# Kernel tuning notes

Hardware: AMD Instinct MI355X
Metric: run time of the kernel (lower is better)

The kernel has to match this reference:

```python
import jax, jax.numpy as jnp
import numpy as np

B, T, C = 2, 2048, 1024
E, F = 8, 1024        # n_experts, expert ffn dim
FS = 2048             # shared expert ffn dim
TOP_K = 2


def setup_inputs() -> dict:
    key = jax.random.key(0)
    ks = jax.random.split(key, 6)
    s = lambda *d: 1.0 / np.sqrt(d[-1])
    return {
        "hidden_tensor": jax.random.normal(ks[0], (B, T, C), jnp.float32),
        "w_router": jax.random.normal(ks[1], (E, C), jnp.float32) * s(C),
        "w1_stack": jax.random.normal(ks[2], (E, F, C), jnp.float32) * s(C),
        "w2_stack": jax.random.normal(ks[3], (E, C, F), jnp.float32) * s(F),
        "ws1": jax.random.normal(ks[4], (FS, C), jnp.float32) * s(C),
        "ws2": jax.random.normal(ks[5], (C, FS), jnp.float32) * s(FS),
    }


def reference(hidden_tensor, w_router, w1_stack, w2_stack, ws1, ws2):
    Bb, Tt, Cc = hidden_tensor.shape
    x = hidden_tensor.reshape(-1, Cc)                      # (t, C)
    t = x.shape[0]

    # --- router: softmax over experts, top-k, renormalize ---
    logits = x @ w_router.T                                # (t, E)
    probs = jax.nn.softmax(logits, axis=-1)
    expert_weight, expert_idx = jax.lax.top_k(probs, TOP_K)  # (t, k)
    expert_weight = expert_weight / jnp.sum(expert_weight, axis=-1, keepdims=True)

    # --- dispatch: stable sort token-expert pairs by expert id ---
    flat_e = expert_idx.reshape(-1)                        # (t*k,)
    order = jnp.argsort(flat_e, stable=True)
    sorted_e = flat_e[order]
    flat_tok = jnp.repeat(jnp.arange(t), TOP_K)
    sorted_tok = flat_tok[order]
    sorted_w = expert_weight.reshape(-1)[order]

    counts = jnp.bincount(sorted_e, length=E)              # (E,)
    offsets = jnp.concatenate([jnp.zeros((1,), counts.dtype), jnp.cumsum(counts)])
    local_pos = jnp.arange(t * TOP_K) - offsets[sorted_e]  # position within expert bin

    cap = t * TOP_K  # static capacity (>= true cnt_max), padding rows stay zero
    binned = jnp.zeros((E, cap, Cc), x.dtype).at[sorted_e, local_pos].set(x[sorted_tok])

    # --- grouped expert FFN with squared-ReLU ---
    inter = jnp.einsum('ecd,efd->ecf', binned, w1_stack)   # (E, cap, F)
    inter = jnp.square(jax.nn.relu(inter))
    outb = jnp.einsum('ecf,edf->ecd', inter, w2_stack)     # (E, cap, C)

    # --- combine: gather back, weight, scatter-add to tokens ---
    flat_out = outb[sorted_e, local_pos] * sorted_w[:, None]
    moe_out = jnp.zeros((t, Cc), x.dtype).at[sorted_tok].add(flat_out)
    moe_out = moe_out.reshape(Bb, Tt, Cc)

    # --- shared expert on residual (squared-ReLU MLP) ---
    sh = jnp.square(jax.nn.relu(jnp.einsum('btc,fc->btf', hidden_tensor, ws1)))
    shared_out = jnp.einsum('btf,cf->btc', sh, ws2)

    return shared_out + moe_out
```

## Files before the change

### kernel.cpp

```cpp
#include <hip/hip_runtime.h>
#include <math.h>

typedef unsigned short u16;
typedef unsigned int u32;

typedef __attribute__((ext_vector_type(8))) short bf16x8;
typedef __attribute__((ext_vector_type(4))) float f32x4;

__device__ __forceinline__ u16 f2bf(float f) {
  union { float f; u32 u; } v; v.f = f;
  u32 r = v.u + 0x7FFFu + ((v.u >> 16) & 1u);
  return (u16)(r >> 16);
}
__device__ __forceinline__ float bf2f(u16 h) {
  union { u32 u; float f; } v; v.u = ((u32)h) << 16; return v.f;
}

typedef const u32 __attribute__((address_space(1)))* gas1_t;
typedef u32 __attribute__((address_space(3)))* las3_t;

__device__ __forceinline__ void gload16(const void* g, void* l) {
  __builtin_amdgcn_global_load_lds((gas1_t)g, (las3_t)l, 16, 0, 0);
}

struct Tile { int kind; int g0; int n0; int e; };

__global__ __launch_bounds__(256) void convert_weights(
    const float4* __restrict__ w1, const float4* __restrict__ w2,
    const float4* __restrict__ s1, const float4* __restrict__ s2,
    ushort4* __restrict__ o1, ushort4* __restrict__ o2,
    ushort4* __restrict__ o3, ushort4* __restrict__ o4) {
  size_t i = (size_t)blockIdx.x * 256 + threadIdx.x;
  const size_t n1 = 2097152, n2 = 2097152, n3 = 524288;
  float4 v; ushort4* o; size_t j;
  if (i < n1)              { v = w1[i];            o = o1; j = i; }
  else if (i < n1+n2)      { v = w2[i-n1];         o = o2; j = i-n1; }
  else if (i < n1+n2+n3)   { v = s1[i-n1-n2];      o = o3; j = i-n1-n2; }
  else                     { v = s2[i-n1-n2-n3];   o = o4; j = i-n1-n2-n3; }
  ushort4 r; r.x = f2bf(v.x); r.y = f2bf(v.y); r.z = f2bf(v.z); r.w = f2bf(v.w);
  o[j] = r;
}

__global__ __launch_bounds__(256) void router_kernel(
    const float* __restrict__ x, const float* __restrict__ wr,
    u16* __restrict__ xb, int* __restrict__ tokE, float* __restrict__ tokW) {
  const int wv = threadIdx.x >> 6, lane = threadIdx.x & 63;
  const int tok = blockIdx.x * 4 + wv;
  const float4* xp = (const float4*)(x + (size_t)tok * 1024);
  float4 xv[4];
#pragma unroll
  for (int i = 0; i < 4; ++i) xv[i] = xp[i * 64 + lane];
  ushort4* xo = (ushort4*)xb + (size_t)tok * 256;
#pragma unroll
  for (int i = 0; i < 4; ++i) {
    ushort4 o;
    o.x = f2bf(xv[i].x); o.y = f2bf(xv[i].y); o.z = f2bf(xv[i].z); o.w = f2bf(xv[i].w);
    xo[i * 64 + lane] = o;
  }
  float acc[8];
#pragma unroll
  for (int e = 0; e < 8; ++e) acc[e] = 0.f;
#pragma unroll
  for (int e = 0; e < 8; ++e) {
    const float4* wp = (const float4*)(wr + e * 1024);
#pragma unroll
    for (int i = 0; i < 4; ++i) {
      float4 w4 = wp[i * 64 + lane];
      acc[e] += xv[i].x * w4.x + xv[i].y * w4.y + xv[i].z * w4.z + xv[i].w * w4.w;
    }
  }
#pragma unroll
  for (int m = 32; m > 0; m >>= 1)
#pragma unroll
    for (int e = 0; e < 8; ++e) acc[e] += __shfl_xor(acc[e], m, 64);
  if (lane == 0) {
    int e0 = 0;
#pragma unroll
    for (int e = 1; e < 8; ++e) if (acc[e] > acc[e0]) e0 = e;
    int e1 = (e0 == 0) ? 1 : 0;
#pragma unroll
    for (int e = 0; e < 8; ++e) if (e != e0 && acc[e] > acc[e1]) e1 = e;
    float p1 = __expf(acc[e1] - acc[e0]);
    float w1 = p1 / (1.f + p1);
    float w0 = 1.f - w1;
    tokE[tok * 2] = e0; tokE[tok * 2 + 1] = e1;
    tokW[tok * 2] = w0; tokW[tok * 2 + 1] = w1;
  }
}

__global__ __launch_bounds__(256) void plan_kernel(
    const int* __restrict__ tokE, const float* __restrict__ tokW,
    Tile* __restrict__ upT, Tile* __restrict__ downT,
    int* __restrict__ rowtok, float* __restrict__ roww, int* __restrict__ invrow) {
  const int t = threadIdx.x, lane = t & 63, wv = t >> 6;
  int myE[32];
#pragma unroll
  for (int i = 0; i < 32; ++i) myE[i] = tokE[t * 32 + i];
  int lcnt[8] = {};
#pragma unroll
  for (int i = 0; i < 32; ++i) ++lcnt[myE[i]];

  __shared__ int wtot[8][4];
  __shared__ int aoffS[9];
  __shared__ int etile[72 * 2];
  int excl[8];
#pragma unroll
  for (int e = 0; e < 8; ++e) {
    int v = lcnt[e];
#pragma unroll
    for (int off = 1; off < 64; off <<= 1) {
      int n = __shfl_up(v, (unsigned)off, 64);
      if (lane >= off) v += n;
    }
    if (lane == 63) wtot[e][wv] = v;
    excl[e] = v - lcnt[e];
  }
  __syncthreads();
#pragma unroll
  for (int e = 0; e < 8; ++e)
    for (int w = 0; w < wv; ++w) excl[e] += wtot[e][w];

  if (t == 0) {
    int s = 0, ti = 0;
    for (int e = 0; e < 8; ++e) {
      aoffS[e] = s;
      int cnt = wtot[e][0] + wtot[e][1] + wtot[e][2] + wtot[e][3];
      int tiles = (cnt + 127) >> 7;
      for (int k = 0; k < tiles; ++k) { etile[2 * ti] = e; etile[2 * ti + 1] = s + k * 128; ++ti; }
      s += tiles << 7;
    }
    aoffS[8] = s;
    for (; ti < 72; ++ti) { etile[2 * ti] = -1; etile[2 * ti + 1] = 0; }
  }
  for (int i = t; i < 9216; i += 256) { rowtok[i] = 0; roww[i] = 0.f; }
  __syncthreads();

  for (int i = t; i < 1088; i += 256) {
    int x = i & 7, s = i >> 3;
    Tile tl;
    if (s < 64) {
      int gg = x & 3, nn = x >> 2;
      int gl = s & 7, nl = s >> 3;
      tl.kind = 0; tl.g0 = (gg * 8 + gl) * 128; tl.n0 = (nn * 8 + nl) * 128; tl.e = 0;
    } else {
      int s2_ = s - 64;
      int mg = x & 3, ng = x >> 2;
      int ml = s2_ % 18, nl = s2_ / 18;
      int mi = mg * 18 + ml;
      int e = etile[2 * mi];
      tl.kind = (e < 0) ? -1 : 1; tl.g0 = etile[2 * mi + 1];
      tl.n0 = (ng * 4 + nl) * 128; tl.e = (e < 0) ? 0 : e;
    }
    upT[i] = tl;
  }
  for (int i = t; i < 832; i += 256) {
    int x = i & 7, s = i >> 3;
    Tile tl;
    if (s < 32) {
      int gg = x & 3, nn = x >> 2;
      int gl = s & 7, nl = s >> 3;
      tl.kind = 0; tl.g0 = (gg * 8 + gl) * 128; tl.n0 = (nn * 4 + nl) * 128; tl.e = 0;
    } else {
      int s2_ = s - 32;
      int mg = x & 3, ng = x >> 2;
      int ml = s2_ % 18, nl = s2_ / 18;
      int mi = mg * 18 + ml;
      int e = etile[2 * mi];
      tl.kind = (e < 0) ? -1 : 1; tl.g0 = etile[2 * mi + 1];
      tl.n0 = (ng * 4 + nl) * 128; tl.e = (e < 0) ? 0 : e;
    }
    downT[i] = tl;
  }

  int pos[8];
#pragma unroll
  for (int e = 0; e < 8; ++e) pos[e] = aoffS[e] + excl[e];
#pragma unroll
  for (int i = 0; i < 32; ++i) {
    int idx = t * 32 + i;
    int e = myE[i];
    int g = pos[e]++;
    rowtok[g] = idx >> 1;
    roww[g] = tokW[idx];
    invrow[idx] = g;
  }
}

__global__ __launch_bounds__(256) void combine_kernel(
    const u16* __restrict__ Ym, const int* __restrict__ invrow,
    const float* __restrict__ tokW, float* __restrict__ out) {
  const int t = blockIdx.x;
  const int r0 = invrow[2 * t], r1 = invrow[2 * t + 1];
  const float w0 = tokW[2 * t], w1 = tokW[2 * t + 1];
  const ushort4* y0 = (const ushort4*)(Ym + (size_t)r0 * 1024);
  const ushort4* y1 = (const ushort4*)(Ym + (size_t)r1 * 1024);
  float4* o = (float4*)(out + (size_t)t * 1024);
  const int c = threadIdx.x;
  ushort4 a = y0[c], b = y1[c];
  float4 v = o[c];
  v.x += w0 * bf2f(a.x) + w1 * bf2f(b.x);
  v.y += w0 * bf2f(a.y) + w1 * bf2f(b.y);
  v.z += w0 * bf2f(a.z) + w1 * bf2f(b.z);
  v.w += w0 * bf2f(a.w) + w1 * bf2f(b.w);
  o[c] = v;
}

template <int PHASE>
__global__ __launch_bounds__(256)
void gemm_fused(const Tile* __restrict__ tiles,
                const u16* __restrict__ A0, const u16* __restrict__ B0, void* __restrict__ C0,
                const u16* __restrict__ A1, const u16* __restrict__ B1, void* __restrict__ C1,
                const int* __restrict__ rowtok, const float* __restrict__ roww) {
  __shared__ u16 As[128 * 64];
  __shared__ u16 Bs[128 * 64];

  Tile tm = tiles[blockIdx.x];
  if (tm.kind < 0) return;
  if (PHASE == 2 && tm.kind != 0) return;
  if (PHASE == 3 && tm.kind != 1) return;

  const int tid = threadIdx.x;
  const int lane = tid & 63;
  const int wv = tid >> 6;
  const int wrow = wv >> 1, wcol = wv & 1;

  const u16* A; const u16* B; void* C; int N, K;
  if (tm.kind == 0) {
    A = A0; B = B0; C = C0;
    N = (PHASE == 0) ? 2048 : 1024;
    K = (PHASE == 0) ? 1024 : 2048;
  } else {
    A = A1; B = B1 + ((size_t)tm.e << 20); C = (PHASE == 3) ? C0 : C1;
    N = 1024; K = 1024;
  }
  const int g0 = tm.g0, n0 = tm.n0;

  const u16* aSrc[4];
  const u16* bSrc[4];
  u32 ldsOff[4];
#pragma unroll
  for (int p = 0; p < 4; ++p) {
    int c = p * 256 + tid;
    int row = c >> 3, slot = c & 7;
    int q = (slot - (row >> 1) - 4 * (row & 1)) & 7;
    int arow = g0 + row;
    if (PHASE == 0 && tm.kind == 1) arow = rowtok[arow];
    aSrc[p] = A + (size_t)arow * K + q * 8;
    bSrc[p] = B + (size_t)(n0 + row) * K + q * 8;
    ldsOff[p] = (u32)(p * 256 + wv * 64) * 16u;
  }

  const int fr = lane & 15, fq = lane >> 4;
  const int swBase = (fr >> 1) + 4 * (fr & 1);
  const int sw0 = ((fq + swBase) & 7) * 8;
  const int sw1 = ((fq + 4 + swBase) & 7) * 8;
  const int aRow = (wrow * 64 + fr) * 64;
  const int bRow = (wcol * 64 + fr) * 64;

  f32x4 acc[4][4] = {};

  for (int k0 = 0; k0 < K; k0 += 64) {
#pragma unroll
    for (int p = 0; p < 4; ++p) {
      gload16(aSrc[p] + k0, (char*)As + ldsOff[p]);
      gload16(bSrc[p] + k0, (char*)Bs + ldsOff[p]);
    }
    __syncthreads();
#pragma unroll
    for (int ks = 0; ks < 2; ++ks) {
      const int sw = ks ? sw1 : sw0;
      bf16x8 af[4], bfg[4];
#pragma unroll
      for (int i = 0; i < 4; ++i) af[i] = *(const bf16x8*)&As[aRow + i * 1024 + sw];
#pragma unroll
      for (int j = 0; j < 4; ++j) bfg[j] = *(const bf16x8*)&Bs[bRow + j * 1024 + sw];
#pragma unroll
      for (int i = 0; i < 4; ++i)
#pragma unroll
        for (int j = 0; j < 4; ++j)
          acc[i][j] = __builtin_amdgcn_mfma_f32_16x16x32_bf16(af[i], bfg[j], acc[i][j], 0, 0, 0);
    }
    __syncthreads();
  }

  if (PHASE == 0) {
    u16* O = (u16*)C;
#pragma unroll
    for (int i = 0; i < 4; ++i) {
      int rb = g0 + wrow * 64 + i * 16 + fq * 4;
#pragma unroll
      for (int j = 0; j < 4; ++j) {
        int col = n0 + wcol * 64 + j * 16 + fr;
#pragma unroll
        for (int r = 0; r < 4; ++r) {
          float v = acc[i][j][r];
          v = v > 0.f ? v * v : 0.f;
          O[(size_t)(rb + r) * N + col] = f2bf(v);
        }
      }
    }
  } else if (PHASE == 1) {
    if (tm.kind == 0) {
      float* O = (float*)C;
#pragma unroll
      for (int i = 0; i < 4; ++i) {
        int rb = g0 + wrow * 64 + i * 16 + fq * 4;
#pragma unroll
        for (int j = 0; j < 4; ++j) {
          int col = n0 + wcol * 64 + j * 16 + fr;
#pragma unroll
          for (int r = 0; r < 4; ++r)
            O[(size_t)(rb + r) * N + col] = acc[i][j][r];
        }
      }
    } else {
      u16* O = (u16*)C;
#pragma unroll
      for (int i = 0; i < 4; ++i) {
        int rb = g0 + wrow * 64 + i * 16 + fq * 4;
#pragma unroll
        for (int j = 0; j < 4; ++j) {
          int col = n0 + wcol * 64 + j * 16 + fr;
#pragma unroll
          for (int r = 0; r < 4; ++r)
            O[(size_t)(rb + r) * N + col] = f2bf(acc[i][j][r]);
        }
      }
    }
  } else if (PHASE == 2) {
    float* O = (float*)C;
#pragma unroll
    for (int i = 0; i < 4; ++i) {
      int rb = g0 + wrow * 64 + i * 16 + fq * 4;
#pragma unroll
      for (int j = 0; j < 4; ++j) {
        int col = n0 + wcol * 64 + j * 16 + fr;
#pragma unroll
        for (int r = 0; r < 4; ++r)
          O[(size_t)(rb + r) * N + col] = acc[i][j][r];
      }
    }
  } else {
    float* O = (float*)C;
#pragma unroll
    for (int i = 0; i < 4; ++i) {
      int rb = g0 + wrow * 64 + i * 16 + fq * 4;
#pragma unroll
      for (int r = 0; r < 4; ++r) {
        int tok = rowtok[rb + r];
        float w = roww[rb + r];
#pragma unroll
        for (int j = 0; j < 4; ++j) {
          int col = n0 + wcol * 64 + j * 16 + fr;
          atomicAdd(&O[(size_t)tok * N + col], w * acc[i][j][r]);
        }
      }
    }
  }
}

extern "C" void kernel_launch(void* const* d_in, const int* in_sizes, int n_in,
                              void* d_out, int out_size, void* d_ws, size_t ws_size,
                              hipStream_t stream) {
  const float* x   = (const float*)d_in[0];
  const float* wr  = (const float*)d_in[1];
  const float* w1  = (const float*)d_in[2];
  const float* w2  = (const float*)d_in[3];
  const float* s1  = (const float*)d_in[4];
  const float* s2  = (const float*)d_in[5];
  float* out = (float*)d_out;

  char* p = (char*)d_ws;
  auto alloc = [&](size_t n) { char* r = p; p += (n + 255) & ~(size_t)255; return r; };
  u16* xb   = (u16*)alloc(4096ULL * 1024 * 2);
  u16* w1b  = (u16*)alloc(8ULL * 1024 * 1024 * 2);
  u16* w2b  = (u16*)alloc(8ULL * 1024 * 1024 * 2);
  u16* s1b  = (u16*)alloc(2048ULL * 1024 * 2);
  u16* s2b  = (u16*)alloc(1024ULL * 2048 * 2);
  u16* Hs   = (u16*)alloc(4096ULL * 2048 * 2);
  u16* Hm   = (u16*)alloc(9216ULL * 1024 * 2);
  int* tokE = (int*)alloc(8192 * 4);
  float* tokW = (float*)alloc(8192 * 4);
  int* rowtok = (int*)alloc(9216 * 4);
  float* roww = (float*)alloc(9216 * 4);
  int* invrow = (int*)alloc(8192 * 4);
  Tile* upT   = (Tile*)alloc(1088 * sizeof(Tile));
  Tile* downT = (Tile*)alloc(832 * sizeof(Tile));
  size_t used_base = (size_t)(p - (char*)d_ws);
  u16* Ym = (u16*)p;
  const bool haveYm = (ws_size - used_base) >= 9216ULL * 1024 * 2;

  convert_weights<<<20480, 256, 0, stream>>>(
      (const float4*)w1, (const float4*)w2, (const float4*)s1, (const float4*)s2,
      (ushort4*)w1b, (ushort4*)w2b, (ushort4*)s1b, (ushort4*)s2b);

  router_kernel<<<1024, 256, 0, stream>>>(x, wr, xb, tokE, tokW);
  plan_kernel<<<1, 256, 0, stream>>>(tokE, tokW, upT, downT, rowtok, roww, invrow);

  gemm_fused<0><<<1088, 256, 0, stream>>>(upT, xb, s1b, Hs, xb, w1b, Hm, rowtok, roww);

  if (haveYm) {
    gemm_fused<1><<<832, 256, 0, stream>>>(downT, Hs, s2b, out, Hm, w2b, Ym, rowtok, roww);
    combine_kernel<<<4096, 256, 0, stream>>>(Ym, invrow, tokW, out);
  } else {
    gemm_fused<2><<<832, 256, 0, stream>>>(downT, Hs, s2b, out, Hm, w2b, nullptr, rowtok, roww);
    gemm_fused<3><<<832, 256, 0, stream>>>(downT, Hs, s2b, out, Hm, w2b, nullptr, rowtok, roww);
  }
}
```

Measured before the change: 289.2 us.

## Merge router into weight conversion kernel and split LDS tiles into K-halves

```diff
diff --git a/kernel.cpp b/kernel.cpp
--- a/kernel.cpp
+++ b/kernel.cpp
@@ -25,25 +25,25 @@
 
 struct Tile { int kind; int g0; int n0; int e; };
 
-__global__ __launch_bounds__(256) void convert_weights(
+__global__ __launch_bounds__(256) void prep_kernel(
+    const float* __restrict__ x, const float* __restrict__ wr,
+    u16* __restrict__ xb, int* __restrict__ tokE, float* __restrict__ tokW,
     const float4* __restrict__ w1, const float4* __restrict__ w2,
     const float4* __restrict__ s1, const float4* __restrict__ s2,
     ushort4* __restrict__ o1, ushort4* __restrict__ o2,
     ushort4* __restrict__ o3, ushort4* __restrict__ o4) {
-  size_t i = (size_t)blockIdx.x * 256 + threadIdx.x;
-  const size_t n1 = 2097152, n2 = 2097152, n3 = 524288;
-  float4 v; ushort4* o; size_t j;
-  if (i < n1)              { v = w1[i];            o = o1; j = i; }
-  else if (i < n1+n2)      { v = w2[i-n1];         o = o2; j = i-n1; }
-  else if (i < n1+n2+n3)   { v = s1[i-n1-n2];      o = o3; j = i-n1-n2; }
-  else                     { v = s2[i-n1-n2-n3];   o = o4; j = i-n1-n2-n3; }
-  ushort4 r; r.x = f2bf(v.x); r.y = f2bf(v.y); r.z = f2bf(v.z); r.w = f2bf(v.w);
-  o[j] = r;
-}
-
-__global__ __launch_bounds__(256) void router_kernel(
-    const float* __restrict__ x, const float* __restrict__ wr,
-    u16* __restrict__ xb, int* __restrict__ tokE, float* __restrict__ tokW) {
+  if (blockIdx.x >= 1024) {
+    size_t i = (size_t)(blockIdx.x - 1024) * 256 + threadIdx.x;
+    const size_t n1 = 2097152, n2 = 2097152, n3 = 524288;
+    float4 v; ushort4* o; size_t j;
+    if (i < n1)              { v = w1[i];            o = o1; j = i; }
+    else if (i < n1+n2)      { v = w2[i-n1];         o = o2; j = i-n1; }
+    else if (i < n1+n2+n3)   { v = s1[i-n1-n2];      o = o3; j = i-n1-n2; }
+    else                     { v = s2[i-n1-n2-n3];   o = o4; j = i-n1-n2-n3; }
+    ushort4 r; r.x = f2bf(v.x); r.y = f2bf(v.y); r.z = f2bf(v.z); r.w = f2bf(v.w);
+    o[j] = r;
+    return;
+  }
   const int wv = threadIdx.x >> 6, lane = threadIdx.x & 63;
   const int tok = blockIdx.x * 4 + wv;
   const float4* xp = (const float4*)(x + (size_t)tok * 1024);
@@ -81,10 +81,10 @@
 #pragma unroll
     for (int e = 0; e < 8; ++e) if (e != e0 && acc[e] > acc[e1]) e1 = e;
     float p1 = __expf(acc[e1] - acc[e0]);
-    float w1 = p1 / (1.f + p1);
-    float w0 = 1.f - w1;
+    float w1_ = p1 / (1.f + p1);
+    float w0 = 1.f - w1_;
     tokE[tok * 2] = e0; tokE[tok * 2 + 1] = e1;
-    tokW[tok * 2] = w0; tokW[tok * 2 + 1] = w1;
+    tokW[tok * 2] = w0; tokW[tok * 2 + 1] = w1_;
   }
 }
 
@@ -235,45 +235,44 @@
   }
   const int g0 = tm.g0, n0 = tm.n0;
 
-  const u16* aSrc[4];
-  const u16* bSrc[4];
-  u32 ldsOff[4];
-#pragma unroll
-  for (int p = 0; p < 4; ++p) {
+  const u16* aSrc[2];
+  const u16* bSrc[2];
+#pragma unroll
+  for (int p = 0; p < 2; ++p) {
     int c = p * 256 + tid;
-    int row = c >> 3, slot = c & 7;
-    int q = (slot - (row >> 1) - 4 * (row & 1)) & 7;
+    int row = c >> 2;
+    int q = ((c & 3) - (row >> 1)) & 3;
     int arow = g0 + row;
     if (PHASE == 0 && tm.kind == 1) arow = rowtok[arow];
     aSrc[p] = A + (size_t)arow * K + q * 8;
     bSrc[p] = B + (size_t)(n0 + row) * K + q * 8;
-    ldsOff[p] = (u32)(p * 256 + wv * 64) * 16u;
-  }
+  }
+  const u32 ldsBase = (u32)(wv * 64) * 16u;
 
   const int fr = lane & 15, fq = lane >> 4;
-  const int swBase = (fr >> 1) + 4 * (fr & 1);
-  const int sw0 = ((fq + swBase) & 7) * 8;
-  const int sw1 = ((fq + 4 + swBase) & 7) * 8;
-  const int aRow = (wrow * 64 + fr) * 64;
-  const int bRow = (wcol * 64 + fr) * 64;
+  const int sw = ((fq + (fr >> 1)) & 3) * 8;
+  const int aRd = (wrow * 64 + fr) * 32 + sw;
+  const int bRd = (wcol * 64 + fr) * 32 + sw;
 
   f32x4 acc[4][4] = {};
 
   for (int k0 = 0; k0 < K; k0 += 64) {
 #pragma unroll
-    for (int p = 0; p < 4; ++p) {
-      gload16(aSrc[p] + k0, (char*)As + ldsOff[p]);
-      gload16(bSrc[p] + k0, (char*)Bs + ldsOff[p]);
+    for (int p = 0; p < 2; ++p) {
+      gload16(aSrc[p] + k0,      (char*)As + ldsBase + p * 4096);
+      gload16(bSrc[p] + k0,      (char*)Bs + ldsBase + p * 4096);
+      gload16(aSrc[p] + k0 + 32, (char*)As + ldsBase + p * 4096 + 8192);
+      gload16(bSrc[p] + k0 + 32, (char*)Bs + ldsBase + p * 4096 + 8192);
     }
     __syncthreads();
 #pragma unroll
     for (int ks = 0; ks < 2; ++ks) {
-      const int sw = ks ? sw1 : sw0;
+      const int sb = ks * 4096;
       bf16x8 af[4], bfg[4];
 #pragma unroll
-      for (int i = 0; i < 4; ++i) af[i] = *(const bf16x8*)&As[aRow + i * 1024 + sw];
-#pragma unroll
-      for (int j = 0; j < 4; ++j) bfg[j] = *(const bf16x8*)&Bs[bRow + j * 1024 + sw];
+      for (int i = 0; i < 4; ++i) af[i] = *(const bf16x8*)&As[sb + aRd + i * 512];
+#pragma unroll
+      for (int j = 0; j < 4; ++j) bfg[j] = *(const bf16x8*)&Bs[sb + bRd + j * 512];
 #pragma unroll
       for (int i = 0; i < 4; ++i)
 #pragma unroll
@@ -390,11 +389,11 @@
   u16* Ym = (u16*)p;
   const bool haveYm = (ws_size - used_base) >= 9216ULL * 1024 * 2;
 
-  convert_weights<<<20480, 256, 0, stream>>>(
+  prep_kernel<<<21504, 256, 0, stream>>>(
+      x, wr, xb, tokE, tokW,
       (const float4*)w1, (const float4*)w2, (const float4*)s1, (const float4*)s2,
       (ushort4*)w1b, (ushort4*)w2b, (ushort4*)s1b, (ushort4*)s2b);
 
-  router_kernel<<<1024, 256, 0, stream>>>(x, wr, xb, tokE, tokW);
   plan_kernel<<<1, 256, 0, stream>>>(tokE, tokW, upT, downT, rowtok, roww, invrow);
 
   gemm_fused<0><<<1088, 256, 0, stream>>>(upT, xb, s1b, Hs, xb, w1b, Hm, rowtok, roww);
```

Measured after the change: 283.0 us. 2.2% less time.
